# Kernel optimization log

Measured on AMD Instinct MI355X. Metric: run time of the kernel, lower is better.

Reference implementation:

```python
import jax, jax.numpy as jnp
import numpy as np

N, C_IN, F = 64, 1024, 20          # batch, backbone channels, grid size (640/32)
N_CLASSES = 80
A = 3                               # anchors in this layer (mask [6,7,8])
STRIDE = 32
C = N_CLASSES + 5                   # 85
C_OUT = A * C                       # 255
ANCHORS = np.array([[116.0, 90.0], [156.0, 198.0], [373.0, 326.0]], np.float32) / STRIDE


def setup_inputs() -> dict:
    key = jax.random.key(0)
    k1, k2 = jax.random.split(key)
    xin = jax.random.normal(k1, (N, C_IN, F, F), jnp.float32)
    conv_w = jax.random.normal(k2, (C_OUT, C_IN, 1, 1), jnp.float32) * 0.02
    conv_b = jnp.zeros((C_OUT,), jnp.float32)
    return {"xin": xin, "conv_w": conv_w, "conv_b": conv_b}


def reference(xin, conv_w, conv_b):
    anchors = jnp.asarray(ANCHORS, dtype=xin.dtype)  # [A, 2], grid units
    # 1x1 conv head: [N, C_OUT, F, F]
    out = jax.lax.conv_general_dilated(xin, conv_w, window_strides=(1, 1),
                                       padding="VALID")
    out = out + conv_b[None, :, None, None]
    # [N, A, C, F, F] -> [N, A, F(y), F(x), C]
    out = out.reshape(N, A, C, F, F).transpose(0, 1, 3, 4, 2)

    xy = jax.nn.sigmoid(out[..., :2])       # sigmoid on tx, ty
    wh = out[..., 2:4]                      # raw tw, th
    objcls = jax.nn.sigmoid(out[..., 4:])   # sigmoid on obj + classes

    grid = jnp.arange(F, dtype=xin.dtype)
    px = xy[..., 0] + grid[None, None, None, :]   # + x_shift (varies along last spatial dim)
    py = xy[..., 1] + grid[None, None, :, None]   # + y_shift
    pw = jnp.exp(wh[..., 0]) * anchors[:, 0].reshape(1, A, 1, 1)
    ph = jnp.exp(wh[..., 1]) * anchors[:, 1].reshape(1, A, 1, 1)

    boxes = jnp.stack([px, py, pw, ph], axis=-1) * STRIDE  # back to pixel coords
    pred = jnp.concatenate([boxes, objcls], axis=-1)       # [N, A, F, F, C]
    return pred.reshape(N, -1, C)                           # [N, A*F*F, C]
```

## Files before the change

### kernel.cpp

```cpp
#include <hip/hip_runtime.h>
#include <hip/hip_bf16.h>
#include <math.h>

#define CIN    1024
#define S_TOT  400
#define COUT   255
#define NCH    85
#define NIMG   64
#define SB     16
#define NTHR   256

#define LDS_BYTES 32768

typedef __attribute__((ext_vector_type(8))) short bf16x8;
typedef __attribute__((ext_vector_type(4))) float f32x4;

struct __attribute__((aligned(4))) f4u { float x, y, z, w; };

__device__ __forceinline__ int xOff(int s, int g) {
    return (s << 11) + ((g << 4) ^ (((s >> 1) & 7) << 4));
}

__device__ __forceinline__ unsigned pk2(float a, float b) {
    __hip_bfloat162 h;
    h.x = __float2bfloat16(a);
    h.y = __float2bfloat16(b);
    return *reinterpret_cast<unsigned*>(&h);
}

__device__ __forceinline__ float sigmoidf_(float v) {
    return 1.0f / (1.0f + expf(-v));
}

__global__ __launch_bounds__(256) void w_pre2(const float* __restrict__ w,
                                              unsigned short* __restrict__ wbf) {
    int gidx = blockIdx.x * 256 + threadIdx.x;
    int co = gidx & 255;
    int g  = gidx >> 8;
    union { unsigned short u[8]; bf16x8 v; } pk;
    if (co < COUT) {
        const float* src = w + (size_t)co * CIN + g * 8;
        #pragma unroll
        for (int j = 0; j < 8; ++j) {
            __hip_bfloat16 h = __float2bfloat16(src[j]);
            pk.u[j] = *reinterpret_cast<unsigned short*>(&h);
        }
    } else {
        #pragma unroll
        for (int j = 0; j < 8; ++j) pk.u[j] = 0;
    }
    *reinterpret_cast<bf16x8*>((char*)wbf + ((size_t)(g << 8) + co) * 16) = pk.v;
}

__global__ __launch_bounds__(NTHR, 4) void yolo_mfma4(
    const float* __restrict__ xin,
    const unsigned short* __restrict__ wbf,
    const float* __restrict__ bias,
    float* __restrict__ out)
{
    __shared__ __align__(16) char smem[LDS_BYTES];

    const int sb  = blockIdx.x * SB;
    const int n   = blockIdx.y;
    const int tid = threadIdx.x;
    const int lane = tid & 63;
    const int wid  = tid >> 6;
    const int llo  = lane & 15;
    const int lhi  = lane >> 4;

    #pragma unroll
    for (int p = 0; p < 2; ++p) {
        const int u   = p * 256 + tid;
        const int g_u = u >> 2;
        const int sq  = u & 3;
        const float* src = xin + ((size_t)n * CIN + g_u * 8) * S_TOT + sb + 4 * sq;
        float4 cu[8];
        #pragma unroll
        for (int j = 0; j < 8; ++j) cu[j] = *(const float4*)(src + j * S_TOT);
        const float* cf = (const float*)cu;
        #pragma unroll
        for (int r = 0; r < 4; ++r) {
            union { unsigned u4[4]; bf16x8 v; } rr;
            #pragma unroll
            for (int j = 0; j < 4; ++j)
                rr.u4[j] = pk2(cf[8 * j + r], cf[8 * j + 4 + r]);
            *(bf16x8*)(smem + xOff(4 * sq + r, g_u)) = rr.v;
        }
    }
    __syncthreads();

    f32x4 acc[4] = {};
    const char* wb = (const char*)wbf;
    const int coB = wid * 64 + llo;

    bf16x8 b_c = *(bf16x8*)(smem + xOff(llo, lhi));
    bf16x8 a_c[4];
    #pragma unroll
    for (int mi = 0; mi < 4; ++mi)
        a_c[mi] = *(const bf16x8*)(wb + ((size_t)((lhi << 8) + coB + mi * 16)) * 16);

    #pragma unroll 4
    for (int kk = 0; kk < 31; ++kk) {
        const int gn = (kk + 1) * 4 + lhi;
        bf16x8 b_n = *(bf16x8*)(smem + xOff(llo, gn));
        bf16x8 a_n[4];
        #pragma unroll
        for (int mi = 0; mi < 4; ++mi)
            a_n[mi] = *(const bf16x8*)(wb + ((size_t)((gn << 8) + coB + mi * 16)) * 16);
        #pragma unroll
        for (int mi = 0; mi < 4; ++mi)
            acc[mi] = __builtin_amdgcn_mfma_f32_16x16x32_bf16(a_c[mi], b_c, acc[mi], 0, 0, 0);
        b_c = b_n;
        #pragma unroll
        for (int mi = 0; mi < 4; ++mi) a_c[mi] = a_n[mi];
    }
    #pragma unroll
    for (int mi = 0; mi < 4; ++mi)
        acc[mi] = __builtin_amdgcn_mfma_f32_16x16x32_bf16(a_c[mi], b_c, acc[mi], 0, 0, 0);

    const float anchW[3] = {116.0f, 156.0f, 373.0f};
    const float anchH[3] = {90.0f, 198.0f, 326.0f};

    const int s = sb + llo;
    const float sx = (float)(s % 20);
    const float sy = (float)(s / 20);

    #pragma unroll
    for (int mi = 0; mi < 4; ++mi) {
        const int co0 = wid * 64 + mi * 16 + lhi * 4;
        const int aW  = co0 / NCH;
        const int c0  = co0 - aW * NCH;
        const bool whole = (c0 <= NCH - 4) && (co0 + 3 < COUT);
        float bv[4];
        #pragma unroll
        for (int r = 0; r < 4; ++r)
            bv[r] = (co0 + r < COUT) ? bias[co0 + r] : 0.0f;

        if (whole) {
            float r4[4];
            #pragma unroll
            for (int r = 0; r < 4; ++r) {
                const int c = c0 + r;
                const float v = acc[mi][r] + bv[r];
                float res;
                if (c == 0)      res = (sigmoidf_(v) + sx) * 32.0f;
                else if (c == 1) res = (sigmoidf_(v) + sy) * 32.0f;
                else if (c == 2) res = expf(v) * anchW[aW];
                else if (c == 3) res = expf(v) * anchH[aW];
                else             res = sigmoidf_(v);
                r4[r] = res;
            }
            f4u* p = (f4u*)(out + (size_t)n * 102000 + aW * 34000 + s * 85 + c0);
            f4u val = {r4[0], r4[1], r4[2], r4[3]};
            *p = val;
        } else {
            #pragma unroll
            for (int r = 0; r < 4; ++r) {
                const int co = co0 + r;
                if (co < COUT) {
                    const int a2 = co / NCH;
                    const int c  = co - a2 * NCH;
                    const float v = acc[mi][r] + bv[r];
                    float res;
                    if (c == 0)      res = (sigmoidf_(v) + sx) * 32.0f;
                    else if (c == 1) res = (sigmoidf_(v) + sy) * 32.0f;
                    else if (c == 2) res = expf(v) * anchW[a2];
                    else if (c == 3) res = expf(v) * anchH[a2];
                    else             res = sigmoidf_(v);
                    out[(size_t)n * 102000 + a2 * 34000 + s * 85 + c] = res;
                }
            }
        }
    }
}

extern "C" void kernel_launch(void* const* d_in, const int* in_sizes, int n_in,
                              void* d_out, int out_size, void* d_ws, size_t ws_size,
                              hipStream_t stream) {
    const float* xin  = (const float*)d_in[0];
    const float* w    = (const float*)d_in[1];
    const float* bias = (const float*)d_in[2];
    float* out = (float*)d_out;
    unsigned short* wbf = (unsigned short*)d_ws;

    w_pre2<<<128, 256, 0, stream>>>(w, wbf);
    yolo_mfma4<<<dim3(S_TOT / SB, NIMG), NTHR, 0, stream>>>(xin, wbf, bias, out);
}
```

Before: 72.50 us.

## Prepack input to bf16 in separate pass and load via global_load_lds

Adds an x_pack kernel that converts the fp32 input into a bf16 layout grouped by 8 channels per spatial position, stored in the workspace. The GEMM kernel then fills LDS with direct global-to-LDS 16-byte loads and drops the in-kernel conversion and the swizzled LDS layout. This aims to make the GEMM's input loads contiguous and cut its register and conversion work, at the cost of an extra kernel launch and an additional full write and read of the packed input. The unswizzled LDS layout may also bring back bank conflicts.

```diff
diff --git a/kernel.cpp b/kernel.cpp
--- a/kernel.cpp
+++ b/kernel.cpp
@@ -17,10 +17,6 @@
 
 struct __attribute__((aligned(4))) f4u { float x, y, z, w; };
 
-__device__ __forceinline__ int xOff(int s, int g) {
-    return (s << 11) + ((g << 4) ^ (((s >> 1) & 7) << 4));
-}
-
 __device__ __forceinline__ unsigned pk2(float a, float b) {
     __hip_bfloat162 h;
     h.x = __float2bfloat16(a);
@@ -30,6 +26,13 @@
 
 __device__ __forceinline__ float sigmoidf_(float v) {
     return 1.0f / (1.0f + expf(-v));
+}
+
+__device__ __forceinline__ void gload_lds16(const void* g, void* l) {
+    __builtin_amdgcn_global_load_lds(
+        (const __attribute__((address_space(1))) unsigned int*)g,
+        (__attribute__((address_space(3))) unsigned int*)l,
+        16, 0, 0);
 }
 
 __global__ __launch_bounds__(256) void w_pre2(const float* __restrict__ w,
@@ -52,8 +55,42 @@
     *reinterpret_cast<bf16x8*>((char*)wbf + ((size_t)(g << 8) + co) * 16) = pk.v;
 }
 
-__global__ __launch_bounds__(NTHR, 4) void yolo_mfma4(
-    const float* __restrict__ xin,
+__global__ __launch_bounds__(256) void x_pack(const float* __restrict__ xin,
+                                              unsigned short* __restrict__ xp) {
+    const int n    = blockIdx.y;
+    const int wid  = threadIdx.x >> 6;
+    const int lane = threadIdx.x & 63;
+    const int g    = blockIdx.x * 4 + wid;
+
+    const float* src = xin + ((size_t)n * CIN + g * 8) * S_TOT;
+    union F4 { float4 v; float f[4]; };
+    F4 v[8][2];
+
+    #pragma unroll
+    for (int ci = 0; ci < 8; ++ci) {
+        v[ci][0].v = *(const float4*)(src + ci * S_TOT + lane * 4);
+        if (lane < 36)
+            v[ci][1].v = *(const float4*)(src + ci * S_TOT + (64 + lane) * 4);
+    }
+
+    unsigned short* dst = xp + ((size_t)(n * 128 + g) * S_TOT) * 8;
+    #pragma unroll
+    for (int r = 0; r < 2; ++r) {
+        const int q = r * 64 + lane;
+        if (r == 1 && lane >= 36) break;
+        #pragma unroll
+        for (int sj = 0; sj < 4; ++sj) {
+            union { unsigned u4[4]; bf16x8 b; } rr;
+            #pragma unroll
+            for (int j = 0; j < 4; ++j)
+                rr.u4[j] = pk2(v[2 * j][r].f[sj], v[2 * j + 1][r].f[sj]);
+            *(bf16x8*)(dst + (size_t)(q * 4 + sj) * 8) = rr.b;
+        }
+    }
+}
+
+__global__ __launch_bounds__(NTHR, 4) void yolo_mfma5(
+    const unsigned short* __restrict__ xp,
     const unsigned short* __restrict__ wbf,
     const float* __restrict__ bias,
     float* __restrict__ out)
@@ -68,24 +105,14 @@
     const int llo  = lane & 15;
     const int lhi  = lane >> 4;
 
-    #pragma unroll
-    for (int p = 0; p < 2; ++p) {
-        const int u   = p * 256 + tid;
-        const int g_u = u >> 2;
-        const int sq  = u & 3;
-        const float* src = xin + ((size_t)n * CIN + g_u * 8) * S_TOT + sb + 4 * sq;
-        float4 cu[8];
-        #pragma unroll
-        for (int j = 0; j < 8; ++j) cu[j] = *(const float4*)(src + j * S_TOT);
-        const float* cf = (const float*)cu;
-        #pragma unroll
-        for (int r = 0; r < 4; ++r) {
-            union { unsigned u4[4]; bf16x8 v; } rr;
-            #pragma unroll
-            for (int j = 0; j < 4; ++j)
-                rr.u4[j] = pk2(cf[8 * j + r], cf[8 * j + 4 + r]);
-            *(bf16x8*)(smem + xOff(4 * sq + r, g_u)) = rr.v;
-        }
+    const char* xsrc = (const char*)xp + (size_t)n * 128 * S_TOT * 16;
+    #pragma unroll
+    for (int i = 0; i < 8; ++i) {
+        const int d  = i * 256 + tid;
+        const int g  = d >> 4;
+        const int sp = d & 15;
+        gload_lds16(xsrc + ((size_t)g * S_TOT + sb + sp) * 16,
+                    smem + i * 4096 + wid * 1024);
     }
     __syncthreads();
 
@@ -93,7 +120,7 @@
     const char* wb = (const char*)wbf;
     const int coB = wid * 64 + llo;
 
-    bf16x8 b_c = *(bf16x8*)(smem + xOff(llo, lhi));
+    bf16x8 b_c = *(bf16x8*)(smem + lhi * 256 + llo * 16);
     bf16x8 a_c[4];
     #pragma unroll
     for (int mi = 0; mi < 4; ++mi)
@@ -102,7 +129,7 @@
     #pragma unroll 4
     for (int kk = 0; kk < 31; ++kk) {
         const int gn = (kk + 1) * 4 + lhi;
-        bf16x8 b_n = *(bf16x8*)(smem + xOff(llo, gn));
+        bf16x8 b_n = *(bf16x8*)(smem + gn * 256 + llo * 16);
         bf16x8 a_n[4];
         #pragma unroll
         for (int mi = 0; mi < 4; ++mi)
@@ -182,7 +209,9 @@
     const float* bias = (const float*)d_in[2];
     float* out = (float*)d_out;
     unsigned short* wbf = (unsigned short*)d_ws;
+    unsigned short* xp  = (unsigned short*)((char*)d_ws + 524288);
 
     w_pre2<<<128, 256, 0, stream>>>(w, wbf);
-    yolo_mfma4<<<dim3(S_TOT / SB, NIMG), NTHR, 0, stream>>>(xin, wbf, bias, out);
-}
+    x_pack<<<dim3(32, NIMG), 256, 0, stream>>>(xin, xp);
+    yolo_mfma5<<<dim3(S_TOT / SB, NIMG), NTHR, 0, stream>>>(xp, wbf, bias, out);
+}
```

Result: slower. 90.52 us (+24.8%).
